# Kernel tuning notes

Measured on AMD Instinct MI355X. Metric: run time of the kernel, lower is better.

The kernel has to match this reference:

```python
import jax, jax.numpy as jnp
import numpy as np

N_NODES = 100000
N_EDGES = 3200000


def gcn_conv(x, src, dst, W, b, n):
    # PyG GCNConv: add self-loops, symmetric normalization, scatter-add to dst.
    loops = jnp.arange(n)
    s = jnp.concatenate([src, loops])
    d = jnp.concatenate([dst, loops])
    h = x @ W                                   # [N, out]
    deg = jnp.zeros((n,), h.dtype).at[d].add(1.0)
    dinv = jnp.where(deg > 0, jax.lax.rsqrt(deg), 0.0)
    norm = dinv[s] * dinv[d]                    # [E+N]
    msg = h[s] * norm[:, None]                  # gather + scale
    out = jax.ops.segment_sum(msg, d, num_segments=n)
    return out + b


def setup_inputs() -> dict:
    key = jax.random.key(0)
    ks = jax.random.split(key, 10)
    x1 = jax.random.normal(ks[0], (N_NODES, 3), dtype=jnp.float32)
    edge_index1 = jax.random.randint(ks[1], (2, N_EDGES), 0, N_NODES, dtype=jnp.int64 if jax.config.jax_enable_x64 else jnp.int32)
    def lin(k, fi, fo):
        s = 1.0 / np.sqrt(fi)
        kw, kb = jax.random.split(k)
        return (jax.random.uniform(kw, (fi, fo), jnp.float32, -s, s),
                jax.random.uniform(kb, (fo,), jnp.float32, -s, s))
    W11, b11 = lin(ks[2], 3, 32)
    W12, b12 = lin(ks[3], 32, 32)
    W13, b13 = lin(ks[4], 32, 32)
    fc_w, fc_b = lin(ks[5], 32, 1)
    return {"x1": x1, "edge_index1": edge_index1,
            "W11": W11, "b11": b11, "W12": W12, "b12": b12,
            "W13": W13, "b13": b13, "fc_w": fc_w, "fc_b": fc_b}


def reference(x1, edge_index1, W11, b11, W12, b12, W13, b13, fc_w, fc_b):
    n = x1.shape[0]
    src, dst = edge_index1[0], edge_index1[1]
    h = gcn_conv(x1, src, dst, W11, b11, n)
    h = jax.nn.relu(h)
    h = gcn_conv(h, src, dst, W12, b12, n)
    h = jax.nn.relu(h)
    h = gcn_conv(h, src, dst, W13, b13, n)
    h = jax.nn.relu(h)
    return h @ fc_w + fc_b                      # [N, 1]
```

## Files before the change

kernel.cpp:

```cpp
#include <hip/hip_runtime.h>
#include <hip/hip_bf16.h>
#include <hip/hip_fp16.h>


#define RBITS  7
#define RNODES 128
#define SBITS  12
#define SNODES 4096
#define BPS    32
#define SMAX   32
#define CE     4096
#define EPT    16

__global__ void k_init(int S, int B, int capS, int capB,
                       int* __restrict__ gcur1, int* __restrict__ gcur2) {
    int t = blockIdx.x * blockDim.x + threadIdx.x;
    if (t < S) gcur1[t] = t * capS;
    if (t < B) gcur2[t] = t * capB;
}

__global__ void k_bin1(const int* __restrict__ src, const int* __restrict__ dst, int E, int S,
                       int* __restrict__ gcur1, unsigned* __restrict__ binned1) {
    __shared__ int cnt[SMAX * 8];
    __shared__ int repOff[SMAX * 8];
    __shared__ int runS[SMAX];
    int tid = threadIdx.x, rep = tid & 7;
    for (int i = tid; i < SMAX * 8; i += 256) cnt[i] = 0;
    __syncthreads();
    int e0 = blockIdx.x * CE;
    int pk[EPT], rnk[EPT], sup[EPT];
#pragma unroll
    for (int j = 0; j < EPT; j++) {
        int e = e0 + j * 256 + tid;
        if (e < E) {
            int d = __builtin_nontemporal_load(dst + e);
            sup[j] = d >> SBITS;
            pk[j]  = (__builtin_nontemporal_load(src + e) << SBITS) | (d & (SNODES - 1));
            rnk[j] = atomicAdd(&cnt[sup[j] * 8 + rep], 1);
        } else sup[j] = -1;
    }
    __syncthreads();
    if (tid < S) {
        int tot = 0;
#pragma unroll
        for (int r = 0; r < 8; r++) { repOff[tid * 8 + r] = tot; tot += cnt[tid * 8 + r]; }
        runS[tid] = tot ? atomicAdd(&gcur1[tid], tot) : 0;
    }
    __syncthreads();
#pragma unroll
    for (int j = 0; j < EPT; j++)
        if (sup[j] >= 0)
            binned1[runS[sup[j]] + repOff[sup[j] * 8 + rep] + rnk[j]] = (unsigned)pk[j];
}

__global__ void k_bin2(const unsigned* __restrict__ binned1, const int* __restrict__ fillEnd,
                       int S, int capS, int* __restrict__ gcur2, unsigned* __restrict__ binned2) {
    __shared__ int send[SMAX];
    __shared__ int cnt[64 * 4];
    __shared__ int repOff[64 * 4];
    __shared__ int runS[64];
    int tid = threadIdx.x, rep = tid & 3;
    if (tid < S) send[tid] = fillEnd[tid];
    for (int i = tid; i < 64 * 4; i += 256) cnt[i] = 0;
    __syncthreads();
    int i0 = blockIdx.x * CE;
    int s0 = i0 / capS;
    int Sc = S * capS;
    unsigned pk[EPT];
    int rnk[EPT], rb[EPT];
#pragma unroll
    for (int j = 0; j < EPT; j++) {
        int idx = i0 + j * 256 + tid;
        rb[j] = -1;
        if (idx < Sc) {
            int sp = idx / capS;
            if (idx < send[sp]) {
                unsigned p = __builtin_nontemporal_load(binned1 + idx);
                int relB = ((sp - s0) << 5) | ((p >> RBITS) & (BPS - 1));
                pk[j] = p; rb[j] = relB;
                rnk[j] = atomicAdd(&cnt[relB * 4 + rep], 1);
            }
        }
    }
    __syncthreads();
    if (tid < 64) {
        int tot = 0;
#pragma unroll
        for (int r = 0; r < 4; r++) { repOff[tid * 4 + r] = tot; tot += cnt[tid * 4 + r]; }
        int sp = s0 + (tid >> 5);
        if (tot && sp < S) {
            int gb = sp * BPS + (tid & (BPS - 1));
            runS[tid] = atomicAdd(&gcur2[gb], tot);
        }
    }
    __syncthreads();
#pragma unroll
    for (int j = 0; j < EPT; j++)
        if (rb[j] >= 0) {
            unsigned p = pk[j];
            binned2[runS[rb[j]] + repOff[rb[j] * 4 + rep] + rnk[j]] =
                ((p >> SBITS) << RBITS) | (p & (RNODES - 1));
        }
}

__global__ void k_sortb2(const unsigned* __restrict__ binned2, const int* __restrict__ gcur2,
                         int capB, int N, int* __restrict__ ssort,
                         int2* __restrict__ row2, float* __restrict__ dinv) {
    __shared__ int cnt[RNODES];
    __shared__ int loc[RNODES];
    int b = blockIdx.x, tid = threadIdx.x;
    int beg = b * capB, end = gcur2[b];
    if (tid < RNODES) cnt[tid] = 0;
    __syncthreads();
    for (int idx = beg + tid; idx < end; idx += 256)
        atomicAdd(&cnt[__builtin_nontemporal_load(binned2 + idx) & (RNODES - 1)], 1);
    __syncthreads();
    if (tid < RNODES) loc[tid] = cnt[tid];
    __syncthreads();
    for (int off = 1; off < RNODES; off <<= 1) {
        int v = 0;
        if (tid < RNODES && tid >= off) v = loc[tid - off];
        __syncthreads();
        if (tid < RNODES) loc[tid] += v;
        __syncthreads();
    }
    int n0 = b << RBITS;
    if (tid < RNODES) {
        int excl = loc[tid] - cnt[tid];
        loc[tid] = beg + excl;
        int n = n0 + tid;
        if (n < N) {
            row2[n] = make_int2(beg + excl, beg + excl + cnt[tid]);
            dinv[n] = rsqrtf((float)cnt[tid] + 1.0f);
        }
    }
    if (tid < RNODES) cnt[tid] = 0;
    __syncthreads();
    for (int idx = beg + tid; idx < end; idx += 256) {
        unsigned p = __builtin_nontemporal_load(binned2 + idx);
        int dl = (int)(p & (RNODES - 1));
        int r  = atomicAdd(&cnt[dl], 1);
        ssort[loc[dl] + r] = (int)(p >> RBITS);
    }
}

__global__ void k_prep1(const float* __restrict__ x, const float* __restrict__ dinv,
                        float4* __restrict__ p4, int N) {
    int n = blockIdx.x * blockDim.x + threadIdx.x;
    if (n >= N) return;
    float di = dinv[n];
    p4[n] = make_float4(x[n * 3] * di, x[n * 3 + 1] * di, x[n * 3 + 2] * di, 0.f);
}

__global__ void k_l1g(const int2* __restrict__ row2, const int* __restrict__ ssort,
                      const float4* __restrict__ p4, const float* __restrict__ dinv,
                      const float* __restrict__ W1, const float* __restrict__ b1,
                      const float* __restrict__ W2, __half* __restrict__ g2, int N) {
    __shared__ float sW1[96];
    __shared__ float sb1[32];
    __shared__ float sW2[1024];
    __shared__ float sh1[256];
    int tid = threadIdx.x;
    for (int i = tid; i < 1024; i += 256) sW2[i] = W2[i];
    if (tid < 96) sW1[tid] = W1[tid];
    if (tid < 32) sb1[tid] = b1[tid];
    __syncthreads();
    int t = blockIdx.x * 256 + tid;
    int n = t >> 5, c = t & 31;
    bool active = (n < N);
    float ax = 0.f, ay = 0.f, az = 0.f;
    float di = 0.f;
    if (active) {
        int2 r = row2[n];
        for (int idx = r.x + c; idx < r.y; idx += 32) {
            float4 q = p4[__builtin_nontemporal_load(ssort + idx)];
            ax += q.x; ay += q.y; az += q.z;
        }
    }
#pragma unroll
    for (int off = 16; off; off >>= 1) {
        ax += __shfl_xor(ax, off, 32);
        ay += __shfl_xor(ay, off, 32);
        az += __shfl_xor(az, off, 32);
    }
    float h1 = 0.f;
    if (active) {
        float4 me = p4[n];
        di = dinv[n];
        ax = di * (ax + me.x); ay = di * (ay + me.y); az = di * (az + me.z);
        h1 = fmaxf(ax * sW1[c] + ay * sW1[32 + c] + az * sW1[64 + c] + sb1[c], 0.f);
    }
    sh1[tid] = h1;
    __syncthreads();
    if (!active) return;
    const float* hr = sh1 + (tid >> 5) * 32;
    float acc = 0.f;
#pragma unroll
    for (int k = 0; k < 32; k++) acc += hr[k] * sW2[k * 32 + c];
    g2[(size_t)n * 32 + c] = __float2half_rn(acc * di);
}

__global__ void k_agg16(const int2* __restrict__ row2, const int* __restrict__ ssort,
                        const __half2* __restrict__ g2, const float* __restrict__ dinv,
                        const float* __restrict__ bias, float* __restrict__ h, int N) {
    int t = blockIdx.x * blockDim.x + threadIdx.x;
    int n = t >> 4, l = t & 15;
    if (n >= N) return;
    int2 r = row2[n];
    int beg = r.x, end = r.y;
    float ax = 0.f, ay = 0.f, bx = 0.f, by = 0.f;
    float cx = 0.f, cy = 0.f, dx = 0.f, dy = 0.f;
    float ex = 0.f, ey = 0.f, fx = 0.f, fy = 0.f;
    float gx = 0.f, gy = 0.f, hx = 0.f, hy = 0.f;
    int base = beg;
    int m = end - base; if (m > 16) m = 16;
    int myS = (m > 0 && l < m) ? __builtin_nontemporal_load(ssort + base + l) : 0;
    while (base < end) {
        int nbase = base + 16;
        int nm = end - nbase; if (nm > 16) nm = 16;
        int nS = (nm > 0 && l < nm) ? __builtin_nontemporal_load(ssort + nbase + l) : 0;
        int i = 0;
        for (; i + 8 <= m; i += 8) {
            int s0 = __shfl(myS, i,     16);
            int s1 = __shfl(myS, i + 1, 16);
            int s2 = __shfl(myS, i + 2, 16);
            int s3 = __shfl(myS, i + 3, 16);
            int s4 = __shfl(myS, i + 4, 16);
            int s5 = __shfl(myS, i + 5, 16);
            int s6 = __shfl(myS, i + 6, 16);
            int s7 = __shfl(myS, i + 7, 16);
            float2 q0 = __half22float2(g2[(size_t)s0 * 16 + l]);
            float2 q1 = __half22float2(g2[(size_t)s1 * 16 + l]);
            float2 q2 = __half22float2(g2[(size_t)s2 * 16 + l]);
            float2 q3 = __half22float2(g2[(size_t)s3 * 16 + l]);
            float2 q4 = __half22float2(g2[(size_t)s4 * 16 + l]);
            float2 q5 = __half22float2(g2[(size_t)s5 * 16 + l]);
            float2 q6 = __half22float2(g2[(size_t)s6 * 16 + l]);
            float2 q7 = __half22float2(g2[(size_t)s7 * 16 + l]);
            ax += q0.x; ay += q0.y;
            bx += q1.x; by += q1.y;
            cx += q2.x; cy += q2.y;
            dx += q3.x; dy += q3.y;
            ex += q4.x; ey += q4.y;
            fx += q5.x; fy += q5.y;
            gx += q6.x; gy += q6.y;
            hx += q7.x; hy += q7.y;
        }
        for (; i + 4 <= m; i += 4) {
            int s0 = __shfl(myS, i,     16);
            int s1 = __shfl(myS, i + 1, 16);
            int s2 = __shfl(myS, i + 2, 16);
            int s3 = __shfl(myS, i + 3, 16);
            float2 q0 = __half22float2(g2[(size_t)s0 * 16 + l]);
            float2 q1 = __half22float2(g2[(size_t)s1 * 16 + l]);
            float2 q2 = __half22float2(g2[(size_t)s2 * 16 + l]);
            float2 q3 = __half22float2(g2[(size_t)s3 * 16 + l]);
            ax += q0.x; ay += q0.y;
            bx += q1.x; by += q1.y;
            cx += q2.x; cy += q2.y;
            dx += q3.x; dy += q3.y;
        }
        for (; i < m; i++) {
            int s = __shfl(myS, i, 16);
            float2 q = __half22float2(g2[(size_t)s * 16 + l]);
            ax += q.x; ay += q.y;
        }
        base = nbase; m = nm; myS = nS;
    }
    float2 self = __half22float2(g2[(size_t)n * 16 + l]);
    float sx = (((ax + bx) + (cx + dx)) + ((ex + fx) + (gx + hx))) + self.x;
    float sy = (((ay + by) + (cy + dy)) + ((ey + fy) + (gy + hy))) + self.y;
    float di = dinv[n];
    int c0 = l * 2;
    float2 o = make_float2(fmaxf(di * sx + bias[c0], 0.f),
                           fmaxf(di * sy + bias[c0 + 1], 0.f));
    double od; __builtin_memcpy(&od, &o, 8);
    __builtin_nontemporal_store(od, (double*)(h + (size_t)n * 32 + c0));
}

__global__ void k_gemv32h(const float* __restrict__ h, const float* __restrict__ W,
                          const float* __restrict__ dinv, __half* __restrict__ g, int N) {
    __shared__ float sW[1024];
    __shared__ float sh[256];
    int tid = threadIdx.x;
    for (int i = tid; i < 1024; i += 256) sW[i] = W[i];
    int t = blockIdx.x * 256 + tid;
    if (t < N * 32) sh[tid] = h[t];
    __syncthreads();
    int n = t >> 5, c = t & 31;
    if (n >= N) return;
    const float* hr = sh + (tid >> 5) * 32;
    float acc = 0.f;
#pragma unroll
    for (int k = 0; k < 32; k++) acc += hr[k] * sW[k * 32 + c];
    g[t] = __float2half_rn(acc * dinv[n]);
}

__global__ void k_agg16_fc(const int2* __restrict__ row2, const int* __restrict__ ssort,
                           const __half2* __restrict__ g2, const float* __restrict__ dinv,
                           const float* __restrict__ bias, const float* __restrict__ fcw,
                           const float* __restrict__ fcb, float* __restrict__ out, int N) {
    int t = blockIdx.x * blockDim.x + threadIdx.x;
    int n = t >> 4, l = t & 15;
    if (n >= N) return;
    int2 r = row2[n];
    int beg = r.x, end = r.y;
    float ax = 0.f, ay = 0.f, bx = 0.f, by = 0.f;
    float cx = 0.f, cy = 0.f, dx = 0.f, dy = 0.f;
    float ex = 0.f, ey = 0.f, fx = 0.f, fy = 0.f;
    float gx = 0.f, gy = 0.f, hx = 0.f, hy = 0.f;
    int base = beg;
    int m = end - base; if (m > 16) m = 16;
    int myS = (m > 0 && l < m) ? __builtin_nontemporal_load(ssort + base + l) : 0;
    while (base < end) {
        int nbase = base + 16;
        int nm = end - nbase; if (nm > 16) nm = 16;
        int nS = (nm > 0 && l < nm) ? __builtin_nontemporal_load(ssort + nbase + l) : 0;
        int i = 0;
        for (; i + 8 <= m; i += 8) {
            int s0 = __shfl(myS, i,     16);
            int s1 = __shfl(myS, i + 1, 16);
            int s2 = __shfl(myS, i + 2, 16);
            int s3 = __shfl(myS, i + 3, 16);
            int s4 = __shfl(myS, i + 4, 16);
            int s5 = __shfl(myS, i + 5, 16);
            int s6 = __shfl(myS, i + 6, 16);
            int s7 = __shfl(myS, i + 7, 16);
            float2 q0 = __half22float2(g2[(size_t)s0 * 16 + l]);
            float2 q1 = __half22float2(g2[(size_t)s1 * 16 + l]);
            float2 q2 = __half22float2(g2[(size_t)s2 * 16 + l]);
            float2 q3 = __half22float2(g2[(size_t)s3 * 16 + l]);
            float2 q4 = __half22float2(g2[(size_t)s4 * 16 + l]);
            float2 q5 = __half22float2(g2[(size_t)s5 * 16 + l]);
            float2 q6 = __half22float2(g2[(size_t)s6 * 16 + l]);
            float2 q7 = __half22float2(g2[(size_t)s7 * 16 + l]);
            ax += q0.x; ay += q0.y;
            bx += q1.x; by += q1.y;
            cx += q2.x; cy += q2.y;
            dx += q3.x; dy += q3.y;
            ex += q4.x; ey += q4.y;
            fx += q5.x; fy += q5.y;
            gx += q6.x; gy += q6.y;
            hx += q7.x; hy += q7.y;
        }
        for (; i + 4 <= m; i += 4) {
            int s0 = __shfl(myS, i,     16);
            int s1 = __shfl(myS, i + 1, 16);
            int s2 = __shfl(myS, i + 2, 16);
            int s3 = __shfl(myS, i + 3, 16);
            float2 q0 = __half22float2(g2[(size_t)s0 * 16 + l]);
            float2 q1 = __half22float2(g2[(size_t)s1 * 16 + l]);
            float2 q2 = __half22float2(g2[(size_t)s2 * 16 + l]);
            float2 q3 = __half22float2(g2[(size_t)s3 * 16 + l]);
            ax += q0.x; ay += q0.y;
            bx += q1.x; by += q1.y;
            cx += q2.x; cy += q2.y;
            dx += q3.x; dy += q3.y;
        }
        for (; i < m; i++) {
            int s = __shfl(myS, i, 16);
            float2 q = __half22float2(g2[(size_t)s * 16 + l]);
            ax += q.x; ay += q.y;
        }
        base = nbase; m = nm; myS = nS;
    }
    float2 self = __half22float2(g2[(size_t)n * 16 + l]);
    float sx = (((ax + bx) + (cx + dx)) + ((ex + fx) + (gx + hx))) + self.x;
    float sy = (((ay + by) + (cy + dy)) + ((ey + fy) + (gy + hy))) + self.y;
    float di = dinv[n];
    int c0 = l * 2;
    float v = fmaxf(di * sx + bias[c0], 0.f) * fcw[c0]
            + fmaxf(di * sy + bias[c0 + 1], 0.f) * fcw[c0 + 1];
    v += __shfl_down(v, 8, 16);
    v += __shfl_down(v, 4, 16);
    v += __shfl_down(v, 2, 16);
    v += __shfl_down(v, 1, 16);
    if (l == 0) out[n] = v + fcb[0];
}

extern "C" void kernel_launch(void* const* d_in, const int* in_sizes, int n_in,
                              void* d_out, int out_size, void* d_ws, size_t ws_size,
                              hipStream_t stream) {
    const float* x1  = (const float*)d_in[0];
    const int*   ei  = (const int*)d_in[1];
    const float* W11 = (const float*)d_in[2];
    const float* b11 = (const float*)d_in[3];
    const float* W12 = (const float*)d_in[4];
    const float* b12 = (const float*)d_in[5];
    const float* W13 = (const float*)d_in[6];
    const float* b13 = (const float*)d_in[7];
    const float* fcw = (const float*)d_in[8];
    const float* fcb = (const float*)d_in[9];
    float* out = (float*)d_out;

    const int N = in_sizes[0] / 3;
    const int E = in_sizes[1] / 2;
    const int* src = ei;
    const int* dst = ei + E;

    const int B = (N + RNODES - 1) / RNODES;
    const int S = (N + SNODES - 1) / SNODES;
    const int capS = E / S + E / S / 16 + 1024;
    const int capB = E / B + E / B / 4 + 256;
    const size_t NC = (size_t)N * 32;

    float4*   p4      = (float4*)d_ws;
    __half*   g       = (__half*)(p4 + N);
    int2*     row2    = (int2*)(g + NC);
    float*    dinv    = (float*)(row2 + N);
    int*      gcur1   = (int*)(dinv + N);
    int*      gcur2   = gcur1 + 32;
    unsigned* binned1 = (unsigned*)(gcur2 + 800);
    unsigned* binned2 = binned1 + (size_t)S * capS;
    int*      ssort   = (int*)(binned2 + (size_t)B * capB);
    float*    h       = (float*)binned1;

    dim3 blk(256);
    dim3 grid_nc(((int)NC + 255) / 256);
    dim3 grid_n((N + 255) / 256);
    dim3 grid_n16(((N * 16) + 255) / 256);
    dim3 grid_e((E + CE - 1) / CE);
    dim3 grid_sc((S * capS + CE - 1) / CE);
    dim3 grid_b(B);

    k_init<<<dim3((B + 255) / 256), blk, 0, stream>>>(S, B, capS, capB, gcur1, gcur2);
    k_bin1<<<grid_e, blk, 0, stream>>>(src, dst, E, S, gcur1, binned1);
    k_bin2<<<grid_sc, blk, 0, stream>>>(binned1, gcur1, S, capS, gcur2, binned2);
    k_sortb2<<<grid_b, blk, 0, stream>>>(binned2, gcur2, capB, N, ssort, row2, dinv);

    k_prep1<<<grid_n, blk, 0, stream>>>(x1, dinv, p4, N);
    k_l1g<<<grid_nc, blk, 0, stream>>>(row2, ssort, p4, dinv, W11, b11, W12, g, N);

    k_agg16<<<grid_n16, blk, 0, stream>>>(row2, ssort, (const __half2*)g, dinv, b12, h, N);
    k_gemv32h<<<grid_nc, blk, 0, stream>>>(h, W13, dinv, g, N);

    k_agg16_fc<<<grid_n16, blk, 0, stream>>>(row2, ssort, (const __half2*)g, dinv, b13, fcw, fcb, out, N);
}
```

Baseline: 225.8 us.

## Fuse layer-2 aggregation with layer-3 GEMV and fold prep into sort kernel

Merges the layer-2 neighbor aggregation with the following 32x32 transform, so the relu'd hidden state stays in shared memory and is never written to or re-read from global memory as fp32. The transformed half-precision features go to a separate buffer that reuses the binned1 workspace. It also folds the per-node x*dinv prep into the sort kernel that computes dinv, dropping one launch. The cost is extra shared memory and a block barrier in the gather kernel, which may lower occupancy for a latency-bound gather.

```diff
diff --git a/kernel.cpp b/kernel.cpp
--- a/kernel.cpp
+++ b/kernel.cpp
@@ -105,7 +105,8 @@
 
 __global__ void k_sortb2(const unsigned* __restrict__ binned2, const int* __restrict__ gcur2,
                          int capB, int N, int* __restrict__ ssort,
-                         int2* __restrict__ row2, float* __restrict__ dinv) {
+                         int2* __restrict__ row2, float* __restrict__ dinv,
+                         const float* __restrict__ x, float4* __restrict__ p4) {
     __shared__ int cnt[RNODES];
     __shared__ int loc[RNODES];
     int b = blockIdx.x, tid = threadIdx.x;
@@ -131,7 +132,10 @@
         int n = n0 + tid;
         if (n < N) {
             row2[n] = make_int2(beg + excl, beg + excl + cnt[tid]);
-            dinv[n] = rsqrtf((float)cnt[tid] + 1.0f);
+            float dv = rsqrtf((float)cnt[tid] + 1.0f);
+            dinv[n] = dv;
+            p4[n] = make_float4(x[n * 3] * dv, x[n * 3 + 1] * dv,
+                                x[n * 3 + 2] * dv, 0.f);
         }
     }
     if (tid < RNODES) cnt[tid] = 0;
@@ -142,14 +146,6 @@
         int r  = atomicAdd(&cnt[dl], 1);
         ssort[loc[dl] + r] = (int)(p >> RBITS);
     }
-}
-
-__global__ void k_prep1(const float* __restrict__ x, const float* __restrict__ dinv,
-                        float4* __restrict__ p4, int N) {
-    int n = blockIdx.x * blockDim.x + threadIdx.x;
-    if (n >= N) return;
-    float di = dinv[n];
-    p4[n] = make_float4(x[n * 3] * di, x[n * 3 + 1] * di, x[n * 3 + 2] * di, 0.f);
 }
 
 __global__ void k_l1g(const int2* __restrict__ row2, const int* __restrict__ ssort,
@@ -200,100 +196,101 @@
     g2[(size_t)n * 32 + c] = __float2half_rn(acc * di);
 }
 
-__global__ void k_agg16(const int2* __restrict__ row2, const int* __restrict__ ssort,
-                        const __half2* __restrict__ g2, const float* __restrict__ dinv,
-                        const float* __restrict__ bias, float* __restrict__ h, int N) {
-    int t = blockIdx.x * blockDim.x + threadIdx.x;
+__global__ void k_agg16g(const int2* __restrict__ row2, const int* __restrict__ ssort,
+                         const __half2* __restrict__ g2, const float* __restrict__ dinv,
+                         const float* __restrict__ bias, const float* __restrict__ W3,
+                         __half* __restrict__ gout, int N) {
+    __shared__ float sW[1024];
+    __shared__ float sh[16 * 33];
+    int tid = threadIdx.x;
+    for (int i = tid; i < 1024; i += 256) sW[i] = W3[i];
+    int t = blockIdx.x * 256 + tid;
     int n = t >> 4, l = t & 15;
-    if (n >= N) return;
-    int2 r = row2[n];
-    int beg = r.x, end = r.y;
-    float ax = 0.f, ay = 0.f, bx = 0.f, by = 0.f;
-    float cx = 0.f, cy = 0.f, dx = 0.f, dy = 0.f;
-    float ex = 0.f, ey = 0.f, fx = 0.f, fy = 0.f;
-    float gx = 0.f, gy = 0.f, hx = 0.f, hy = 0.f;
-    int base = beg;
-    int m = end - base; if (m > 16) m = 16;
-    int myS = (m > 0 && l < m) ? __builtin_nontemporal_load(ssort + base + l) : 0;
-    while (base < end) {
-        int nbase = base + 16;
-        int nm = end - nbase; if (nm > 16) nm = 16;
-        int nS = (nm > 0 && l < nm) ? __builtin_nontemporal_load(ssort + nbase + l) : 0;
-        int i = 0;
-        for (; i + 8 <= m; i += 8) {
-            int s0 = __shfl(myS, i,     16);
-            int s1 = __shfl(myS, i + 1, 16);
-            int s2 = __shfl(myS, i + 2, 16);
-            int s3 = __shfl(myS, i + 3, 16);
-            int s4 = __shfl(myS, i + 4, 16);
-            int s5 = __shfl(myS, i + 5, 16);
-            int s6 = __shfl(myS, i + 6, 16);
-            int s7 = __shfl(myS, i + 7, 16);
-            float2 q0 = __half22float2(g2[(size_t)s0 * 16 + l]);
-            float2 q1 = __half22float2(g2[(size_t)s1 * 16 + l]);
-            float2 q2 = __half22float2(g2[(size_t)s2 * 16 + l]);
-            float2 q3 = __half22float2(g2[(size_t)s3 * 16 + l]);
-            float2 q4 = __half22float2(g2[(size_t)s4 * 16 + l]);
-            float2 q5 = __half22float2(g2[(size_t)s5 * 16 + l]);
-            float2 q6 = __half22float2(g2[(size_t)s6 * 16 + l]);
-            float2 q7 = __half22float2(g2[(size_t)s7 * 16 + l]);
-            ax += q0.x; ay += q0.y;
-            bx += q1.x; by += q1.y;
-            cx += q2.x; cy += q2.y;
-            dx += q3.x; dy += q3.y;
-            ex += q4.x; ey += q4.y;
-            fx += q5.x; fy += q5.y;
-            gx += q6.x; gy += q6.y;
-            hx += q7.x; hy += q7.y;
-        }
-        for (; i + 4 <= m; i += 4) {
-            int s0 = __shfl(myS, i,     16);
-            int s1 = __shfl(myS, i + 1, 16);
-            int s2 = __shfl(myS, i + 2, 16);
-            int s3 = __shfl(myS, i + 3, 16);
-            float2 q0 = __half22float2(g2[(size_t)s0 * 16 + l]);
-            float2 q1 = __half22float2(g2[(size_t)s1 * 16 + l]);
-            float2 q2 = __half22float2(g2[(size_t)s2 * 16 + l]);
-            float2 q3 = __half22float2(g2[(size_t)s3 * 16 + l]);
-            ax += q0.x; ay += q0.y;
-            bx += q1.x; by += q1.y;
-            cx += q2.x; cy += q2.y;
-            dx += q3.x; dy += q3.y;
-        }
-        for (; i < m; i++) {
-            int s = __shfl(myS, i, 16);
-            float2 q = __half22float2(g2[(size_t)s * 16 + l]);
-            ax += q.x; ay += q.y;
-        }
-        base = nbase; m = nm; myS = nS;
-    }
-    float2 self = __half22float2(g2[(size_t)n * 16 + l]);
-    float sx = (((ax + bx) + (cx + dx)) + ((ex + fx) + (gx + hx))) + self.x;
-    float sy = (((ay + by) + (cy + dy)) + ((ey + fy) + (gy + hy))) + self.y;
-    float di = dinv[n];
     int c0 = l * 2;
-    float2 o = make_float2(fmaxf(di * sx + bias[c0], 0.f),
-                           fmaxf(di * sy + bias[c0 + 1], 0.f));
-    double od; __builtin_memcpy(&od, &o, 8);
-    __builtin_nontemporal_store(od, (double*)(h + (size_t)n * 32 + c0));
-}
-
-__global__ void k_gemv32h(const float* __restrict__ h, const float* __restrict__ W,
-                          const float* __restrict__ dinv, __half* __restrict__ g, int N) {
-    __shared__ float sW[1024];
-    __shared__ float sh[256];
-    int tid = threadIdx.x;
-    for (int i = tid; i < 1024; i += 256) sW[i] = W[i];
-    int t = blockIdx.x * 256 + tid;
-    if (t < N * 32) sh[tid] = h[t];
-    __syncthreads();
-    int n = t >> 5, c = t & 31;
-    if (n >= N) return;
-    const float* hr = sh + (tid >> 5) * 32;
-    float acc = 0.f;
-#pragma unroll
-    for (int k = 0; k < 32; k++) acc += hr[k] * sW[k * 32 + c];
-    g[t] = __float2half_rn(acc * dinv[n]);
+    bool act = (n < N);
+    float di = 0.f;
+    if (act) {
+        int2 r = row2[n];
+        int beg = r.x, end = r.y;
+        float ax = 0.f, ay = 0.f, bx = 0.f, by = 0.f;
+        float cx = 0.f, cy = 0.f, dx = 0.f, dy = 0.f;
+        float ex = 0.f, ey = 0.f, fx = 0.f, fy = 0.f;
+        float gx = 0.f, gy = 0.f, hx = 0.f, hy = 0.f;
+        int base = beg;
+        int m = end - base; if (m > 16) m = 16;
+        int myS = (m > 0 && l < m) ? __builtin_nontemporal_load(ssort + base + l) : 0;
+        while (base < end) {
+            int nbase = base + 16;
+            int nm = end - nbase; if (nm > 16) nm = 16;
+            int nS = (nm > 0 && l < nm) ? __builtin_nontemporal_load(ssort + nbase + l) : 0;
+            int i = 0;
+            for (; i + 8 <= m; i += 8) {
+                int s0 = __shfl(myS, i,     16);
+                int s1 = __shfl(myS, i + 1, 16);
+                int s2 = __shfl(myS, i + 2, 16);
+                int s3 = __shfl(myS, i + 3, 16);
+                int s4 = __shfl(myS, i + 4, 16);
+                int s5 = __shfl(myS, i + 5, 16);
+                int s6 = __shfl(myS, i + 6, 16);
+                int s7 = __shfl(myS, i + 7, 16);
+                float2 q0 = __half22float2(g2[(size_t)s0 * 16 + l]);
+                float2 q1 = __half22float2(g2[(size_t)s1 * 16 + l]);
+                float2 q2 = __half22float2(g2[(size_t)s2 * 16 + l]);
+                float2 q3 = __half22float2(g2[(size_t)s3 * 16 + l]);
+                float2 q4 = __half22float2(g2[(size_t)s4 * 16 + l]);
+                float2 q5 = __half22float2(g2[(size_t)s5 * 16 + l]);
+                float2 q6 = __half22float2(g2[(size_t)s6 * 16 + l]);
+                float2 q7 = __half22float2(g2[(size_t)s7 * 16 + l]);
+                ax += q0.x; ay += q0.y;
+                bx += q1.x; by += q1.y;
+                cx += q2.x; cy += q2.y;
+                dx += q3.x; dy += q3.y;
+                ex += q4.x; ey += q4.y;
+                fx += q5.x; fy += q5.y;
+                gx += q6.x; gy += q6.y;
+                hx += q7.x; hy += q7.y;
+            }
+            for (; i + 4 <= m; i += 4) {
+                int s0 = __shfl(myS, i,     16);
+                int s1 = __shfl(myS, i + 1, 16);
+                int s2 = __shfl(myS, i + 2, 16);
+                int s3 = __shfl(myS, i + 3, 16);
+                float2 q0 = __half22float2(g2[(size_t)s0 * 16 + l]);
+                float2 q1 = __half22float2(g2[(size_t)s1 * 16 + l]);
+                float2 q2 = __half22float2(g2[(size_t)s2 * 16 + l]);
+                float2 q3 = __half22float2(g2[(size_t)s3 * 16 + l]);
+                ax += q0.x; ay += q0.y;
+                bx += q1.x; by += q1.y;
+                cx += q2.x; cy += q2.y;
+                dx += q3.x; dy += q3.y;
+            }
+            for (; i < m; i++) {
+                int s = __shfl(myS, i, 16);
+                float2 q = __half22float2(g2[(size_t)s * 16 + l]);
+                ax += q.x; ay += q.y;
+            }
+            base = nbase; m = nm; myS = nS;
+        }
+        float2 self = __half22float2(g2[(size_t)n * 16 + l]);
+        float sx = (((ax + bx) + (cx + dx)) + ((ex + fx) + (gx + hx))) + self.x;
+        float sy = (((ay + by) + (cy + dy)) + ((ey + fy) + (gy + hy))) + self.y;
+        di = dinv[n];
+        int nn = tid >> 4;
+        sh[nn * 33 + c0]     = fmaxf(di * sx + bias[c0], 0.f);
+        sh[nn * 33 + c0 + 1] = fmaxf(di * sy + bias[c0 + 1], 0.f);
+    }
+    __syncthreads();
+    if (!act) return;
+    const float* hr = sh + (tid >> 4) * 33;
+    float a0 = 0.f, a1 = 0.f;
+#pragma unroll
+    for (int k = 0; k < 32; k++) {
+        float hv = hr[k];
+        float2 w = *(const float2*)(sW + k * 32 + c0);
+        a0 += hv * w.x; a1 += hv * w.y;
+    }
+    __half2 o = __floats2half2_rn(a0 * di, a1 * di);
+    *(__half2*)(gout + (size_t)n * 32 + c0) = o;
 }
 
 __global__ void k_agg16_fc(const int2* __restrict__ row2, const int* __restrict__ ssort,
@@ -413,11 +410,10 @@
     unsigned* binned1 = (unsigned*)(gcur2 + 800);
     unsigned* binned2 = binned1 + (size_t)S * capS;
     int*      ssort   = (int*)(binned2 + (size_t)B * capB);
-    float*    h       = (float*)binned1;
+    __half*   gout    = (__half*)binned1;
 
     dim3 blk(256);
     dim3 grid_nc(((int)NC + 255) / 256);
-    dim3 grid_n((N + 255) / 256);
     dim3 grid_n16(((N * 16) + 255) / 256);
     dim3 grid_e((E + CE - 1) / CE);
     dim3 grid_sc((S * capS + CE - 1) / CE);
@@ -426,13 +422,11 @@
     k_init<<<dim3((B + 255) / 256), blk, 0, stream>>>(S, B, capS, capB, gcur1, gcur2);
     k_bin1<<<grid_e, blk, 0, stream>>>(src, dst, E, S, gcur1, binned1);
     k_bin2<<<grid_sc, blk, 0, stream>>>(binned1, gcur1, S, capS, gcur2, binned2);
-    k_sortb2<<<grid_b, blk, 0, stream>>>(binned2, gcur2, capB, N, ssort, row2, dinv);
-
-    k_prep1<<<grid_n, blk, 0, stream>>>(x1, dinv, p4, N);
+    k_sortb2<<<grid_b, blk, 0, stream>>>(binned2, gcur2, capB, N, ssort, row2, dinv, x1, p4);
+
     k_l1g<<<grid_nc, blk, 0, stream>>>(row2, ssort, p4, dinv, W11, b11, W12, g, N);
 
-    k_agg16<<<grid_n16, blk, 0, stream>>>(row2, ssort, (const __half2*)g, dinv, b12, h, N);
-    k_gemv32h<<<grid_nc, blk, 0, stream>>>(h, W13, dinv, g, N);
-
-    k_agg16_fc<<<grid_n16, blk, 0, stream>>>(row2, ssort, (const __half2*)g, dinv, b13, fcw, fcb, out, N);
-}
+    k_agg16g<<<grid_n16, blk, 0, stream>>>(row2, ssort, (const __half2*)g, dinv, b12, W13, gout, N);
+
+    k_agg16_fc<<<grid_n16, blk, 0, stream>>>(row2, ssort, (const __half2*)gout, dinv, b13, fcw, fcb, out, N);
+}
```

Result: faster. 211.7 us (-6.2%).
